# Optimization experiments

Hardware: AMD Instinct MI355X
Metric: run time of the kernel (lower is better)

Reference implementation:

```python
import jax, jax.numpy as jnp
import numpy as np

B, T, E = 8, 2048, 512  # batch, seq_len, dim (single head, head_dim == dim)
EPS = 1e-3


def setup_inputs() -> dict:
    key = jax.random.key(0)
    ks = jax.random.split(key, 6)
    s = E ** -0.5  # scale proj weights like nn.Linear init so exp(k) stays finite
    return {
        "x": jax.random.normal(ks[0], (B, E, T), jnp.float32),
        "toep_weight": jax.random.normal(ks[1], (1, T), jnp.float32),
        "q_w": jax.random.normal(ks[2], (E, E), jnp.float32) * s,
        "q_b": jnp.zeros((E,), jnp.float32),
        "k_w": jax.random.normal(ks[3], (E, E), jnp.float32) * s,
        "k_b": jnp.zeros((E,), jnp.float32),
        "v_w": jax.random.normal(ks[4], (E, E), jnp.float32) * s,
        "v_b": jnp.zeros((E,), jnp.float32),
        "o_w": jax.random.normal(ks[5], (E, E), jnp.float32) * s,
        "o_b": jnp.zeros((E,), jnp.float32),
    }


def reference(x, toep_weight, q_w, q_b, k_w, k_b, v_w, v_b, o_w, o_b):
    # x: (B, E, T) -> (B, T, E)
    xt = jnp.transpose(x, (0, 2, 1))
    q = xt @ q_w.T + q_b
    k = xt @ k_w.T + k_b
    v = xt @ v_w.T + v_b
    # feature maps: softmax(q) * d^-1/2 , exp(k); v scaled by per-position Toeplitz weight
    q = jax.nn.softmax(q, axis=-1) * (E ** -0.5)
    k = jnp.exp(k)
    v = v * toep_weight[0][:, None]  # (T,1) broadcast over (B,T,E)
    # causal linear attention: running outer-product state S (B,E,E) and key-sum z (B,E)
    qs = jnp.transpose(q, (1, 0, 2))  # (T, B, E)
    kk = jnp.transpose(k, (1, 0, 2))
    vv = jnp.transpose(v, (1, 0, 2))

    def step(carry, inp):
        S, z = carry
        qt, kt, vt = inp  # each (B, E)
        S = S + kt[:, :, None] * vt[:, None, :]  # cumulative k v^T
        z = z + kt                                # cumulative key sum
        d = jnp.maximum(jnp.sum(z * qt, axis=-1), EPS)  # clamp then reciprocal
        out = jnp.einsum('bd,bde->be', qt, S) / d[:, None]
        return (S, z), out

    S0 = jnp.zeros((B, E, E), q.dtype)
    z0 = jnp.zeros((B, E), q.dtype)
    _, outs = jax.lax.scan(step, (S0, z0), (qs, kk, vv))  # outs: (T, B, E)
    attn = jnp.transpose(outs, (1, 0, 2))  # (B, T, E)
    return attn @ o_w.T + o_b
```

## Files before the change

kernel.cpp:

```cpp
#include <hip/hip_runtime.h>
#include <hip/hip_bf16.h>
#include <math.h>
#include <stdint.h>

#define B_ 8
#define T_ 2048
#define E_ 512
#define CCH 256
#define NC_ 8
#define EPS_ 1e-3f
#define QSCALE 0.044194173824159216f

typedef __attribute__((ext_vector_type(8))) short short8;
typedef __attribute__((ext_vector_type(4))) float f32x4;
typedef __hip_bfloat16 bf16_t;

__device__ __forceinline__ short f2bs(float x) {
    bf16_t h = __float2bfloat16(x);
    return __builtin_bit_cast(short, h);
}
__device__ __forceinline__ float bs2f(short s) {
    bf16_t h = __builtin_bit_cast(bf16_t, s);
    return __bfloat162float(h);
}

__device__ __forceinline__ void async16(const void* g, void* l) {
    __builtin_amdgcn_global_load_lds(
        (const __attribute__((address_space(1))) unsigned int*)(unsigned long long)(uintptr_t)g,
        (__attribute__((address_space(3))) unsigned int*)(unsigned int)(uintptr_t)l,
        16, 0, 0);
}

__device__ __forceinline__ void gemm128(const short* __restrict__ Ag, int lda,
                                        const short* __restrict__ Bg, int ldb, int K,
                                        short* L, f32x4 acc[4][4],
                                        int wm, int wn, int wq, int lane) {
    int m16 = lane & 15, quad = lane >> 4;
    int r16 = lane & 15, c4 = quad * 8;
    int nstep = K >> 5;
    __syncthreads();
    #pragma unroll
    for (int w = 0; w < 2; ++w) {
        int win = wq + w * 4;
        async16(Ag + (size_t)(win * 16 + r16) * lda + c4, L + win * 512);
        async16(Bg + (size_t)(win * 16 + r16) * ldb + c4, L + 4096 + win * 512);
    }
    for (int i = 0; i < nstep; ++i) {
        int cur = (i & 1) << 13;
        int nxt = 8192 - cur;
        __syncthreads();
        if (i + 1 < nstep) {
            int k0 = (i + 1) << 5;
            #pragma unroll
            for (int w = 0; w < 2; ++w) {
                int win = wq + w * 4;
                async16(Ag + (size_t)(win * 16 + r16) * lda + k0 + c4, L + nxt + win * 512);
                async16(Bg + (size_t)(win * 16 + r16) * ldb + k0 + c4, L + nxt + 4096 + win * 512);
            }
        }
        const short* Ac = L + cur;
        const short* Bc = L + cur + 4096;
        short8 a[4], b[4];
        #pragma unroll
        for (int t = 0; t < 4; ++t)
            a[t] = *(const short8*)(Ac + (wm + t * 16) * 32 + quad * 128 + m16 * 8);
        #pragma unroll
        for (int t = 0; t < 4; ++t)
            b[t] = *(const short8*)(Bc + (wn + t * 16) * 32 + quad * 128 + m16 * 8);
        #pragma unroll
        for (int t = 0; t < 4; ++t)
            #pragma unroll
            for (int j = 0; j < 4; ++j)
                acc[t][j] = __builtin_amdgcn_mfma_f32_16x16x32_bf16(a[t], b[j], acc[t][j], 0, 0, 0);
    }
}

#define GEMM_PROLOG \
    int tid = threadIdx.x, lane = tid & 63, wq = tid >> 6; \
    int wm = (wq & 1) * 64, wn = (wq >> 1) * 64; \
    int m16 = lane & 15, quad = lane >> 4; \
    (void)tid; \
    f32x4 acc[4][4]; \
    { f32x4 zz = {0.f, 0.f, 0.f, 0.f}; \
      for (int i = 0; i < 4; ++i) for (int j = 0; j < 4; ++j) acc[i][j] = zz; }

__global__ void prep_kernel(const float* __restrict__ qw, const float* __restrict__ kw,
                            const float* __restrict__ vw, const float* __restrict__ ow,
                            short* __restrict__ wbf,
                            const float* __restrict__ x, short* __restrict__ xbf) {
    int bid = blockIdx.x;
    int tid = threadIdx.x;
    if (bid < 512) {
        size_t idx8 = ((size_t)bid * 256 + tid) * 8;
        int sel = (int)(idx8 >> 18);
        size_t off = idx8 & ((1u << 18) - 1);
        const float* src = sel == 0 ? qw : sel == 1 ? kw : sel == 2 ? vw : ow;
        const float4* sp = (const float4*)(src + off);
        float4 a = sp[0], b = sp[1];
        short8 g;
        g[0] = f2bs(a.x); g[1] = f2bs(a.y); g[2] = f2bs(a.z); g[3] = f2bs(a.w);
        g[4] = f2bs(b.x); g[5] = f2bs(b.y); g[6] = f2bs(b.z); g[7] = f2bs(b.w);
        *(short8*)(wbf + idx8) = g;
        return;
    }
    bid -= 512;
    __shared__ __align__(16) float S[64][68];
    int t0 = (bid & 31) * 64, e0 = ((bid >> 5) & 7) * 64, b = bid >> 8;
    const float* src = x + ((size_t)b * E_ + e0) * T_ + t0;
    short* dst = xbf + ((size_t)b * T_ + t0) * E_ + e0;
    #pragma unroll
    for (int p = 0; p < 2; ++p) {
        int el = p * 32 + (tid >> 3), tc = (tid & 7) * 8;
        const float4* sp = (const float4*)(src + (size_t)el * T_ + tc);
        *(float4*)&S[el][tc] = sp[0];
        *(float4*)&S[el][tc + 4] = sp[1];
    }
    __syncthreads();
    #pragma unroll
    for (int p = 0; p < 2; ++p) {
        int tl = p * 32 + (tid >> 3), ec = (tid & 7) * 8;
        short8 g;
        #pragma unroll
        for (int j = 0; j < 8; ++j) g[j] = f2bs(S[ec + j][tl]);
        *(short8*)(dst + (size_t)tl * E_ + ec) = g;
    }
}

__global__ void transpose_bf_kernel(const short* __restrict__ k, const short* __restrict__ v,
                                    short* __restrict__ kT, short* __restrict__ vT) {
    __shared__ __align__(16) short S[64][72];
    int tid = threadIdx.x;
    int t0 = blockIdx.x * 64, e0 = blockIdx.y * 64;
    int b = blockIdx.z >> 1, which = blockIdx.z & 1;
    const short* src = (which ? v : k) + ((size_t)b * T_ + t0) * E_ + e0;
    short* dst = (which ? vT : kT) + ((size_t)b * E_ + e0) * T_ + t0;
    #pragma unroll
    for (int p = 0; p < 2; ++p) {
        int tl = p * 32 + (tid >> 3), ec = (tid & 7) * 8;
        *(short8*)&S[tl][ec] = *(const short8*)(src + (size_t)tl * E_ + ec);
    }
    __syncthreads();
    #pragma unroll
    for (int p = 0; p < 2; ++p) {
        int er = p * 32 + (tid >> 3), tc = (tid & 7) * 8;
        short8 g;
        #pragma unroll
        for (int j = 0; j < 8; ++j) g[j] = S[tc + j][er];
        *(short8*)(dst + (size_t)er * T_ + tc) = g;
    }
}

__global__ __launch_bounds__(256) void proj_qkv_kernel(
    const short* __restrict__ xbf, const short* __restrict__ wbf,
    const float* __restrict__ qb, const float* __restrict__ kb, const float* __restrict__ vb,
    const float* __restrict__ toep,
    bf16_t* __restrict__ qraw, bf16_t* __restrict__ kout, bf16_t* __restrict__ vout) {
    __shared__ __align__(16) short L[16384];
    GEMM_PROLOG
    int t0 = blockIdx.x * 128, i0 = blockIdx.y * 128;
    int b = blockIdx.z / 3, sel = blockIdx.z % 3;
    const short* Ag = xbf + ((size_t)b * T_ + t0) * E_;
    const short* Bg = wbf + (size_t)sel * E_ * E_ + (size_t)i0 * E_;
    gemm128(Ag, E_, Bg, E_, E_, L, acc, wm, wn, wq, lane);
    const float* bias = (sel == 0) ? qb : (sel == 1) ? kb : vb;
    #pragma unroll
    for (int mt = 0; mt < 4; ++mt)
        #pragma unroll
        for (int r = 0; r < 4; ++r) {
            int t = t0 + wm + mt * 16 + quad * 4 + r;
            size_t rowoff = ((size_t)b * T_ + t) * E_;
            float tw = toep[t];
            #pragma unroll
            for (int nt = 0; nt < 4; ++nt) {
                int col = i0 + wn + nt * 16 + m16;
                float vv = acc[mt][nt][r] + bias[col];
                if (sel == 0) qraw[rowoff + col] = __float2bfloat16(vv);
                else if (sel == 1) kout[rowoff + col] = __float2bfloat16(expf(vv));
                else vout[rowoff + col] = __float2bfloat16(vv * tw);
            }
        }
}

__global__ void softmax_ksum_kernel(const bf16_t* __restrict__ qraw, bf16_t* __restrict__ qbf,
                                    const bf16_t* __restrict__ k, float* __restrict__ ks) {
    int bid = blockIdx.x, tid = threadIdx.x;
    if (bid >= B_ * T_) {
        int r = bid - B_ * T_;
        int bc = r >> 1, b = bc >> 3, c = bc & 7;
        int e = (r & 1) * 256 + tid;
        const bf16_t* kp = k + ((size_t)b * T_ + (size_t)c * CCH) * E_ + e;
        float s = 0.f;
        for (int t = 0; t < CCH; ++t) s += __bfloat162float(kp[(size_t)t * E_]);
        ks[(size_t)bc * E_ + e] = s;
        return;
    }
    __shared__ float red[256];
    const bf16_t* p = qraw + (size_t)bid * E_;
    float v0 = __bfloat162float(p[tid]), v1 = __bfloat162float(p[tid + 256]);
    red[tid] = fmaxf(v0, v1);
    __syncthreads();
    for (int s = 128; s > 0; s >>= 1) { if (tid < s) red[tid] = fmaxf(red[tid], red[tid + s]); __syncthreads(); }
    float m = red[0];
    __syncthreads();
    float e0 = expf(v0 - m), e1 = expf(v1 - m);
    red[tid] = e0 + e1;
    __syncthreads();
    for (int s = 128; s > 0; s >>= 1) { if (tid < s) red[tid] += red[tid + s]; __syncthreads(); }
    float inv = QSCALE / red[0];
    qbf[(size_t)bid * E_ + tid] = __float2bfloat16(e0 * inv);
    qbf[(size_t)bid * E_ + tid + 256] = __float2bfloat16(e1 * inv);
}

__global__ __launch_bounds__(256) void kvp_kernel(
    const short* __restrict__ vT, const short* __restrict__ kT, bf16_t* __restrict__ KV,
    const short* __restrict__ qbf, const short* __restrict__ kbf, bf16_t* __restrict__ P) {
    __shared__ __align__(16) short L[16384];
    int bid = blockIdx.x;
    if (bid < 1024) {
        GEMM_PROLOG
        int ev0 = (bid & 3) * 128, ek0 = ((bid >> 2) & 3) * 128;
        int bc = bid >> 4, b = bc >> 3, c = bc & 7;
        const short* Ag = vT + ((size_t)b * E_ + ev0) * T_ + c * CCH;
        const short* Bg = kT + ((size_t)b * E_ + ek0) * T_ + c * CCH;
        gemm128(Ag, T_, Bg, T_, CCH, L, acc, wm, wn, wq, lane);
        #pragma unroll
        for (int mt = 0; mt < 4; ++mt)
            #pragma unroll
            for (int r = 0; r < 4; ++r) {
                int ev = ev0 + wm + mt * 16 + quad * 4 + r;
                #pragma unroll
                for (int nt = 0; nt < 4; ++nt) {
                    int ek = ek0 + wn + nt * 16 + m16;
                    KV[((size_t)bc * E_ + ev) * E_ + ek] = __float2bfloat16(acc[mt][nt][r]);
                }
            }
        return;
    }
    bid -= 1024;
    int tj0 = (bid & 1) * 128, ti0 = ((bid >> 1) & 1) * 128;
    int bc = bid >> 2, b = bc >> 3, c = bc & 7;
    short* Pp = (short*)P + (size_t)bc * CCH * CCH;
    if (tj0 > ti0) {
        short8 z8 = {0, 0, 0, 0, 0, 0, 0, 0};
        for (int i = threadIdx.x; i < 128 * 128 / 8; i += 256) {
            int row = i >> 4, colc = (i * 8) & 127;
            *(short8*)(Pp + (size_t)(ti0 + row) * CCH + tj0 + colc) = z8;
        }
        return;
    }
    GEMM_PROLOG
    const short* Ag = qbf + ((size_t)b * T_ + c * CCH + ti0) * E_;
    const short* Bg = kbf + ((size_t)b * T_ + c * CCH + tj0) * E_;
    gemm128(Ag, E_, Bg, E_, E_, L, acc, wm, wn, wq, lane);
    #pragma unroll
    for (int mt = 0; mt < 4; ++mt)
        #pragma unroll
        for (int r = 0; r < 4; ++r) {
            int row = ti0 + wm + mt * 16 + quad * 4 + r;
            #pragma unroll
            for (int nt = 0; nt < 4; ++nt) {
                int col = tj0 + wn + nt * 16 + m16;
                float vv = (col <= row) ? acc[mt][nt][r] : 0.f;
                ((bf16_t*)Pp)[(size_t)row * CCH + col] = __float2bfloat16(vv);
            }
        }
}

__global__ void scan2_kernel(short* __restrict__ KV, float* __restrict__ ks) {
    int bid = blockIdx.x, tid = threadIdx.x;
    if (bid < 1024) {
        int gid = bid * 256 + tid;
        int b = gid >> 15;
        size_t idx = (size_t)(gid & 32767) * 8;
        short* p = KV + (size_t)b * NC_ * E_ * E_ + idx;
        float run[8] = {0.f, 0.f, 0.f, 0.f, 0.f, 0.f, 0.f, 0.f};
        #pragma unroll
        for (int c = 0; c < NC_; ++c) {
            short8 t8 = *(short8*)p;
            short8 o8;
            #pragma unroll
            for (int j = 0; j < 8; ++j) {
                float tv = bs2f(t8[j]);
                o8[j] = f2bs(run[j]);
                run[j] += tv;
            }
            *(short8*)p = o8;
            p += (size_t)E_ * E_;
        }
        return;
    }
    int gid = (bid - 1024) * 256 + tid;
    int b = gid >> 9, idx = gid & (E_ - 1);
    float run = 0.f;
    float* p = ks + (size_t)b * NC_ * E_ + idx;
    for (int c = 0; c < NC_; ++c) { float t = *p; *p = run; run += t; p += E_; }
}

__global__ void denom_kernel(const bf16_t* __restrict__ qbf, const float* __restrict__ z,
                             const bf16_t* __restrict__ P, float* __restrict__ invd) {
    __shared__ float red[256];
    int row = blockIdx.x, tid = threadIdx.x;
    int b = row >> 11, t = row & (T_ - 1);
    int c = t >> 8, tl = t & 255;
    const bf16_t* qr = qbf + (size_t)row * E_;
    const float* zr = z + ((size_t)(b * NC_ + c)) * E_;
    const bf16_t* Pr = P + (((size_t)(b * NC_ + c)) * CCH + tl) * CCH;
    float s = __bfloat162float(qr[tid]) * zr[tid]
            + __bfloat162float(qr[tid + 256]) * zr[tid + 256]
            + __bfloat162float(Pr[tid]);
    red[tid] = s;
    __syncthreads();
    for (int st = 128; st > 0; st >>= 1) { if (tid < st) red[tid] += red[tid + st]; __syncthreads(); }
    if (tid == 0) invd[row] = 1.f / fmaxf(red[0], EPS_);
}

__global__ __launch_bounds__(256) void attnout_kernel(
    const short* __restrict__ qbf, const short* __restrict__ KV,
    const short* __restrict__ P, const short* __restrict__ vT,
    const float* __restrict__ invd, bf16_t* __restrict__ attn) {
    __shared__ __align__(16) short L[16384];
    GEMM_PROLOG
    int t0 = blockIdx.x * 128, i0 = blockIdx.y * 128, b = blockIdx.z;
    int c = t0 >> 8, tl0 = t0 & 255, bc = b * NC_ + c;
    gemm128(qbf + ((size_t)b * T_ + t0) * E_, E_,
            KV + ((size_t)bc * E_ + i0) * E_, E_, E_, L, acc, wm, wn, wq, lane);
    gemm128(P + ((size_t)bc * CCH + tl0) * CCH, CCH,
            vT + ((size_t)b * E_ + i0) * T_ + c * CCH, T_, CCH, L, acc, wm, wn, wq, lane);
    #pragma unroll
    for (int mt = 0; mt < 4; ++mt)
        #pragma unroll
        for (int r = 0; r < 4; ++r) {
            int t = t0 + wm + mt * 16 + quad * 4 + r;
            float sc = invd[(size_t)b * T_ + t];
            #pragma unroll
            for (int nt = 0; nt < 4; ++nt) {
                int col = i0 + wn + nt * 16 + m16;
                attn[((size_t)b * T_ + t) * E_ + col] = __float2bfloat16(acc[mt][nt][r] * sc);
            }
        }
}

__global__ __launch_bounds__(256) void outproj_kernel(
    const short* __restrict__ attn, const short* __restrict__ wbf_o,
    const float* __restrict__ ob, float* __restrict__ out) {
    __shared__ __align__(16) short L[16384];
    GEMM_PROLOG
    int t0 = blockIdx.x * 128, i0 = blockIdx.y * 128, b = blockIdx.z;
    gemm128(attn + ((size_t)b * T_ + t0) * E_, E_,
            wbf_o + (size_t)i0 * E_, E_, E_, L, acc, wm, wn, wq, lane);
    #pragma unroll
    for (int mt = 0; mt < 4; ++mt)
        #pragma unroll
        for (int r = 0; r < 4; ++r) {
            int t = t0 + wm + mt * 16 + quad * 4 + r;
            #pragma unroll
            for (int nt = 0; nt < 4; ++nt) {
                int col = i0 + wn + nt * 16 + m16;
                out[((size_t)b * T_ + t) * E_ + col] = acc[mt][nt][r] + ob[col];
            }
        }
}

extern "C" void kernel_launch(void* const* d_in, const int* in_sizes, int n_in,
                              void* d_out, int out_size, void* d_ws, size_t ws_size,
                              hipStream_t stream) {
    const float* x    = (const float*)d_in[0];
    const float* toep = (const float*)d_in[1];
    const float* q_w  = (const float*)d_in[2];
    const float* q_b  = (const float*)d_in[3];
    const float* k_w  = (const float*)d_in[4];
    const float* k_b  = (const float*)d_in[5];
    const float* v_w  = (const float*)d_in[6];
    const float* v_b  = (const float*)d_in[7];
    const float* o_w  = (const float*)d_in[8];
    const float* o_b  = (const float*)d_in[9];

    const size_t NTE = (size_t)B_ * T_ * E_;
    char* base = (char*)d_ws;
    short* xbf  = (short*)base;  base += NTE * 2;
    short* wbf  = (short*)base;  base += (size_t)4 * E_ * E_ * 2;
    short* qraw = (short*)base;  base += NTE * 2;
    short* qbf  = (short*)base;  base += NTE * 2;
    short* kbf  = (short*)base;  base += NTE * 2;
    short* vbf  = (short*)base;  base += NTE * 2;
    short* kT   = (short*)base;  base += NTE * 2;
    short* vT   = (short*)base;  base += NTE * 2;
    short* KV   = (short*)base;  base += (size_t)B_ * NC_ * E_ * E_ * 2;
    short* P    = (short*)base;  base += (size_t)B_ * NC_ * CCH * CCH * 2;
    float* ksum = (float*)base;  base += (size_t)B_ * NC_ * E_ * 4;
    float* invd = (float*)base;  base += (size_t)B_ * T_ * 4;
    short* attn = xbf;
    float* out  = (float*)d_out;

    dim3 blk(256);
    prep_kernel<<<dim3(2560), blk, 0, stream>>>(q_w, k_w, v_w, o_w, wbf, x, xbf);
    proj_qkv_kernel<<<dim3(16, 4, 24), blk, 0, stream>>>(
        xbf, wbf, q_b, k_b, v_b, toep, (bf16_t*)qraw, (bf16_t*)kbf, (bf16_t*)vbf);
    softmax_ksum_kernel<<<dim3(B_ * T_ + 128), blk, 0, stream>>>(
        (const bf16_t*)qraw, (bf16_t*)qbf, (const bf16_t*)kbf, ksum);
    transpose_bf_kernel<<<dim3(32, 8, 16), blk, 0, stream>>>(kbf, vbf, kT, vT);
    kvp_kernel<<<dim3(1280), blk, 0, stream>>>(
        vT, kT, (bf16_t*)KV, qbf, kbf, (bf16_t*)P);
    scan2_kernel<<<dim3(1040), blk, 0, stream>>>(KV, ksum);
    denom_kernel<<<dim3(B_ * T_), blk, 0, stream>>>(
        (const bf16_t*)qbf, ksum, (const bf16_t*)P, invd);
    attnout_kernel<<<dim3(16, 4, 8), blk, 0, stream>>>(
        qbf, KV, P, vT, invd, (bf16_t*)attn);
    outproj_kernel<<<dim3(16, 4, 8), blk, 0, stream>>>(
        attn, wbf + (size_t)3 * E_ * E_, o_b, out);
}
```

Measured before the change: 308.2 us.

## Use XOR-swizzled K=64 LDS tiles in gemm128, drop double buffering

Replaces the double-buffered K=32 tile loop with a single-buffered K=64 tile per iteration, stored in LDS row-major with an XOR swizzle on the 16-byte chunk index. This is meant to avoid LDS bank conflicts on the fragment reads and to halve the number of barrier-separated iterations. In exchange, the next tile's global-to-LDS load no longer overlaps with MFMA work, so each iteration waits for its load to finish.

```diff
diff --git a/kernel.cpp b/kernel.cpp
--- a/kernel.cpp
+++ b/kernel.cpp
@@ -36,42 +36,34 @@
                                         short* L, f32x4 acc[4][4],
                                         int wm, int wn, int wq, int lane) {
     int m16 = lane & 15, quad = lane >> 4;
-    int r16 = lane & 15, c4 = quad * 8;
-    int nstep = K >> 5;
-    __syncthreads();
-    #pragma unroll
-    for (int w = 0; w < 2; ++w) {
-        int win = wq + w * 4;
-        async16(Ag + (size_t)(win * 16 + r16) * lda + c4, L + win * 512);
-        async16(Bg + (size_t)(win * 16 + r16) * ldb + c4, L + 4096 + win * 512);
-    }
-    for (int i = 0; i < nstep; ++i) {
-        int cur = (i & 1) << 13;
-        int nxt = 8192 - cur;
+    int lrow = lane >> 3;
+    int lchunk = (lane & 7) ^ lrow;
+    short* Bl = L + 8192;
+    for (int k0 = 0; k0 < K; k0 += 64) {
         __syncthreads();
-        if (i + 1 < nstep) {
-            int k0 = (i + 1) << 5;
-            #pragma unroll
-            for (int w = 0; w < 2; ++w) {
-                int win = wq + w * 4;
-                async16(Ag + (size_t)(win * 16 + r16) * lda + k0 + c4, L + nxt + win * 512);
-                async16(Bg + (size_t)(win * 16 + r16) * ldb + k0 + c4, L + nxt + 4096 + win * 512);
-            }
-        }
-        const short* Ac = L + cur;
-        const short* Bc = L + cur + 4096;
-        short8 a[4], b[4];
-        #pragma unroll
-        for (int t = 0; t < 4; ++t)
-            a[t] = *(const short8*)(Ac + (wm + t * 16) * 32 + quad * 128 + m16 * 8);
-        #pragma unroll
-        for (int t = 0; t < 4; ++t)
-            b[t] = *(const short8*)(Bc + (wn + t * 16) * 32 + quad * 128 + m16 * 8);
-        #pragma unroll
-        for (int t = 0; t < 4; ++t)
-            #pragma unroll
-            for (int j = 0; j < 4; ++j)
-                acc[t][j] = __builtin_amdgcn_mfma_f32_16x16x32_bf16(a[t], b[j], acc[t][j], 0, 0, 0);
+        #pragma unroll
+        for (int w = 0; w < 4; ++w) {
+            int R = wq * 32 + w * 8;
+            async16(Ag + (size_t)(R + lrow) * lda + k0 + lchunk * 8, L + R * 64);
+            async16(Bg + (size_t)(R + lrow) * ldb + k0 + lchunk * 8, Bl + R * 64);
+        }
+        __syncthreads();
+        #pragma unroll
+        for (int h = 0; h < 2; ++h) {
+            int cs = ((h * 4 + quad) ^ (m16 & 7)) * 8;
+            short8 a[4], b[4];
+            #pragma unroll
+            for (int t = 0; t < 4; ++t)
+                a[t] = *(const short8*)(L + (wm + t * 16 + m16) * 64 + cs);
+            #pragma unroll
+            for (int t = 0; t < 4; ++t)
+                b[t] = *(const short8*)(Bl + (wn + t * 16 + m16) * 64 + cs);
+            #pragma unroll
+            for (int t = 0; t < 4; ++t)
+                #pragma unroll
+                for (int j = 0; j < 4; ++j)
+                    acc[t][j] = __builtin_amdgcn_mfma_f32_16x16x32_bf16(a[t], b[j], acc[t][j], 0, 0, 0);
+        }
     }
 }
 
```

New measurement: 275.5 us. 1.12x faster.
